# Kernel tuning notes

Measured on AMD Instinct MI355X. Metric: run time of the kernel, lower is better.

Reference implementation:

```python
import jax, jax.numpy as jnp
import numpy as np
import math

EMBED_DIM = 4096
NUM_HEADS = 32
NUM_KV_HEADS = 8
HEAD_DIM = EMBED_DIM // NUM_HEADS          # 128
GROUP_SIZE = NUM_HEADS // NUM_KV_HEADS     # 4
KV_DIM = EMBED_DIM // GROUP_SIZE           # 1024
BATCH, SEQ = 1, 2048


def softermax(x, axis=-1):
    # base-2 softmax with max subtraction (Softermax, arXiv:2103.09301)
    m = jnp.max(x, axis=axis, keepdims=True)
    p = jnp.exp2(x - m)
    return p / jnp.sum(p, axis=axis, keepdims=True)


def setup_inputs() -> dict:
    key = jax.random.key(0)
    ks = jax.random.split(key, 9)
    s = 1.0 / math.sqrt(EMBED_DIM)
    return {
        "x": jax.random.normal(ks[0], (BATCH, SEQ, EMBED_DIM), jnp.float32),
        "q_w": jax.random.normal(ks[1], (EMBED_DIM, EMBED_DIM), jnp.float32) * s,
        "q_b": jax.random.normal(ks[2], (EMBED_DIM,), jnp.float32) * s,
        "k_w": jax.random.normal(ks[3], (KV_DIM, EMBED_DIM), jnp.float32) * s,
        "k_b": jax.random.normal(ks[4], (KV_DIM,), jnp.float32) * s,
        "v_w": jax.random.normal(ks[5], (KV_DIM, EMBED_DIM), jnp.float32) * s,
        "v_b": jax.random.normal(ks[6], (KV_DIM,), jnp.float32) * s,
        "o_w": jax.random.normal(ks[7], (EMBED_DIM, EMBED_DIM), jnp.float32) * s,
        "o_b": jax.random.normal(ks[8], (EMBED_DIM,), jnp.float32) * s,
    }


def reference(x, q_w, q_b, k_w, k_b, v_w, v_b, o_w, o_b):
    B, S, E = x.shape
    # projections (torch Linear: y = x @ W.T + b)
    q = (x @ q_w.T + q_b).reshape(B, S, NUM_HEADS, HEAD_DIM).transpose(0, 2, 1, 3)   # [B,H,S,D]
    k = (x @ k_w.T + k_b).reshape(B, S, NUM_KV_HEADS, HEAD_DIM).transpose(0, 2, 1, 3)  # [B,KV,S,D]
    v = (x @ v_w.T + v_b).reshape(B, S, NUM_KV_HEADS, HEAD_DIM).transpose(0, 2, 1, 3)
    # repeat_kv: expand kv heads to num_heads
    k = jnp.repeat(k, GROUP_SIZE, axis=1)  # [B,H,S,D]
    v = jnp.repeat(v, GROUP_SIZE, axis=1)
    scale = 1.0 / math.sqrt(HEAD_DIM)
    attn = jnp.einsum("bhqd,bhkd->bhqk", q, k * scale)
    attn = softermax(attn, axis=-1)
    out = jnp.einsum("bhqk,bhkd->bhqd", attn, v)
    out = out.transpose(0, 2, 1, 3).reshape(B, S, E)
    return out @ o_w.T + o_b
```

## Files before the change

kernel.cpp:

```cpp
#include <hip/hip_runtime.h>
#include <hip/hip_bf16.h>
#include <stdint.h>

#define SEQL 2048
#define EMB 4096
#define KVDIM 1024
#define NHEADS 32
#define HD 128

typedef __attribute__((ext_vector_type(4))) float f32x4;
typedef __attribute__((ext_vector_type(8))) short bf16x8;
typedef unsigned short u16;
typedef unsigned int u32;

__device__ __forceinline__ u16 f2bf(float f) {
  u32 u = __builtin_bit_cast(u32, f);
  u = (u + 0x7FFFu + ((u >> 16) & 1u)) >> 16;
  return (u16)u;
}

__device__ __forceinline__ void gload_lds16(const void* g, void* l) {
  __builtin_amdgcn_global_load_lds(
      (const __attribute__((address_space(1))) void*)g,
      (__attribute__((address_space(3))) void*)l, 16, 0, 0);
}

__global__ __launch_bounds__(256) void k_convert(
    const float* __restrict__ x, const float* __restrict__ qw,
    const float* __restrict__ kw, const float* __restrict__ vw,
    const float* __restrict__ ow, u16* __restrict__ xb, u16* __restrict__ qwb,
    u16* __restrict__ kwb, u16* __restrict__ vwb, u16* __restrict__ owb) {
  const long NCH = 6291456;
  const long stride = (long)gridDim.x * 256;
  for (long c = (long)blockIdx.x * 256 + threadIdx.x; c < NCH; c += stride) {
    long i = c << 3;
    const float* s;
    u16* d;
    long off;
    if (i < 8388608) {
      s = x; d = xb; off = i;
    } else if (i < 25165824) {
      s = qw; d = qwb; off = i - 8388608;
    } else if (i < 29360128) {
      s = kw; d = kwb; off = i - 25165824;
    } else if (i < 33554432) {
      s = vw; d = vwb; off = i - 29360128;
    } else {
      s = ow; d = owb; off = i - 33554432;
    }
    float4 a = *(const float4*)(s + off);
    float4 b = *(const float4*)(s + off + 4);
    bf16x8 o;
    o[0] = f2bf(a.x); o[1] = f2bf(a.y); o[2] = f2bf(a.z); o[3] = f2bf(a.w);
    o[4] = f2bf(b.x); o[5] = f2bf(b.y); o[6] = f2bf(b.z); o[7] = f2bf(b.w);
    *(bf16x8*)(d + off) = o;
  }
}

__device__ __forceinline__ void gemm_core128(const u16* __restrict__ A,
                                             const u16* __restrict__ W, long m0,
                                             long n0, int lda, int ldb, int nkt,
                                             u16* sA, u16* sB, f32x4 acc[4][4]) {
  const int t = threadIdx.x, lane = t & 63, w = t >> 6;
  const int wr = w >> 1, wc = w & 1, r15 = lane & 15, kof = (lane >> 4) * 8;
  auto stage = [&](int buf, int kt) {
    const long k0 = (long)kt * 32;
#pragma unroll
    for (int i = 0; i < 2; ++i) {
      const int L = (i * 256 + t) * 8;
      gload_lds16(A + (m0 + (L >> 5)) * lda + k0 + (L & 31),
                  sA + buf * 4096 + i * 2048 + w * 512);
      gload_lds16(W + (n0 + (L >> 5)) * ldb + k0 + (L & 31),
                  sB + buf * 4096 + i * 2048 + w * 512);
    }
  };
  stage(0, 0);
  __syncthreads();
  int cur = 0;
  for (int kt = 0; kt < nkt; ++kt) {
    if (kt + 1 < nkt) stage(cur ^ 1, kt + 1);
    bf16x8 aF[4], bF[4];
#pragma unroll
    for (int m = 0; m < 4; ++m)
      aF[m] = *(const bf16x8*)(sA + cur * 4096 + (wr * 64 + m * 16 + r15) * 32 + kof);
#pragma unroll
    for (int n = 0; n < 4; ++n)
      bF[n] = *(const bf16x8*)(sB + cur * 4096 + (wc * 64 + n * 16 + r15) * 32 + kof);
#pragma unroll
    for (int m = 0; m < 4; ++m)
#pragma unroll
      for (int n = 0; n < 4; ++n)
        acc[m][n] =
            __builtin_amdgcn_mfma_f32_16x16x32_bf16(aF[m], bF[n], acc[m][n], 0, 0, 0);
    __syncthreads();
    cur ^= 1;
  }
}

__global__ __launch_bounds__(256, 2) void k_gemm_qkv(
    const u16* __restrict__ xb, const u16* __restrict__ qwb,
    const u16* __restrict__ kwb, const u16* __restrict__ vwb,
    const float* __restrict__ qb, const float* __restrict__ kb,
    const float* __restrict__ vb, u16* __restrict__ Q, u16* __restrict__ Kc,
    u16* __restrict__ Vt) {
  __shared__ u16 sA[2 * 4096];
  __shared__ u16 sB[2 * 4096];
  const int nt = blockIdx.x, mt = blockIdx.y;
  const u16* W;
  const float* bias;
  long n0;
  int mode;
  if (nt < 32) {
    W = qwb; bias = qb; n0 = (long)nt * 128; mode = 0;
  } else if (nt < 40) {
    W = kwb; bias = kb; n0 = (long)(nt - 32) * 128; mode = 1;
  } else {
    W = vwb; bias = vb; n0 = (long)(nt - 40) * 128; mode = 2;
  }
  const long m0 = (long)mt * 128;
  f32x4 acc[4][4] = {};
  gemm_core128(xb, W, m0, n0, EMB, EMB, 128, sA, sB, acc);
  const int lane = threadIdx.x & 63, w = threadIdx.x >> 6;
  const int wr = w >> 1, wc = w & 1, r15 = lane & 15, hi = lane >> 4;
#pragma unroll
  for (int n = 0; n < 4; ++n) {
    const long col = n0 + wc * 64 + n * 16 + r15;
    const float bv = bias[col];
#pragma unroll
    for (int m = 0; m < 4; ++m) {
#pragma unroll
      for (int i = 0; i < 4; ++i) {
        const long row = m0 + wr * 64 + m * 16 + hi * 4 + i;
        const float v = acc[m][n][i] + bv;
        if (mode == 0)
          Q[row * EMB + col] = f2bf(v);
        else if (mode == 1)
          Kc[row * KVDIM + col] = f2bf(v);
        else
          Vt[col * SEQL + row] = f2bf(v);
      }
    }
  }
}

__global__ __launch_bounds__(256, 2) void k_attn(const u16* __restrict__ Q,
                                                 const u16* __restrict__ Kc,
                                                 const u16* __restrict__ Vt,
                                                 u16* __restrict__ AO) {
  __shared__ u16 sK[64 * 128];
  __shared__ u16 sV[128 * 64];
  __shared__ u16 sP[4][32 * 72];
  const int h = blockIdx.y, kvh = h >> 2;
  const long q0 = (long)blockIdx.x * 128;
  const int t = threadIdx.x, lane = t & 63, w = t >> 6;
  const int r15 = lane & 15, hi = lane >> 4, kof = hi * 8;
  const float scale = 0.08838834764831845f;

  bf16x8 qf[2][4];
#pragma unroll
  for (int m = 0; m < 2; ++m)
#pragma unroll
    for (int ks = 0; ks < 4; ++ks)
      qf[m][ks] = *(const bf16x8*)(Q + (q0 + w * 32 + m * 16 + r15) * EMB +
                                   h * HD + ks * 32 + kof);

  f32x4 oacc[2][8] = {};
  float mx[2][4], sm[2][4];
#pragma unroll
  for (int m = 0; m < 2; ++m)
#pragma unroll
    for (int i = 0; i < 4; ++i) {
      mx[m][i] = -1e30f;
      sm[m][i] = 0.f;
    }

  for (int tk = 0; tk < 32; ++tk) {
    const long k0 = (long)tk * 64;
    __syncthreads();
#pragma unroll
    for (int i = 0; i < 4; ++i) {
      const int P = (i * 256 + t) * 16;
      const int row = P >> 8;
      const int cb = (P & 255) ^ ((row & 7) << 4);
      gload_lds16(Kc + (k0 + row) * KVDIM + kvh * HD + (cb >> 1),
                  (char*)sK + (i * 256 + w * 64) * 16);
      const int rowv = P >> 7;
      const int cbv = (P & 127) ^ ((rowv & 7) << 4);
      gload_lds16(Vt + (long)(kvh * HD + rowv) * SEQL + k0 + (cbv >> 1),
                  (char*)sV + (i * 256 + w * 64) * 16);
    }
    __syncthreads();
    f32x4 sacc[2][4] = {};
#pragma unroll
    for (int ks = 0; ks < 4; ++ks) {
      bf16x8 bF[4];
#pragma unroll
      for (int n = 0; n < 4; ++n) {
        const int row = n * 16 + r15;
        const int off = (row << 8) + (((ks * 32 + kof) << 1) ^ ((row & 7) << 4));
        bF[n] = *(const bf16x8*)((const char*)sK + off);
      }
#pragma unroll
      for (int m = 0; m < 2; ++m)
#pragma unroll
        for (int n = 0; n < 4; ++n)
          sacc[m][n] = __builtin_amdgcn_mfma_f32_16x16x32_bf16(qf[m][ks], bF[n],
                                                               sacc[m][n], 0, 0, 0);
    }
#pragma unroll
    for (int m = 0; m < 2; ++m) {
#pragma unroll
      for (int i = 0; i < 4; ++i) {
        float tmax = fmaxf(fmaxf(sacc[m][0][i], sacc[m][1][i]),
                           fmaxf(sacc[m][2][i], sacc[m][3][i]));
#pragma unroll
        for (int msk = 1; msk < 16; msk <<= 1)
          tmax = fmaxf(tmax, __shfl_xor(tmax, msk, 64));
        const float nm = fmaxf(mx[m][i], tmax * scale);
        const float corr = exp2f(mx[m][i] - nm);
        mx[m][i] = nm;
        sm[m][i] *= corr;
#pragma unroll
        for (int n = 0; n < 8; ++n) oacc[m][n][i] *= corr;
        float ps = 0.f;
#pragma unroll
        for (int n = 0; n < 4; ++n) {
          const float p = exp2f(sacc[m][n][i] * scale - nm);
          ps += p;
          sP[w][(m * 16 + hi * 4 + i) * 72 + n * 16 + r15] = f2bf(p);
        }
#pragma unroll
        for (int msk = 1; msk < 16; msk <<= 1) ps += __shfl_xor(ps, msk, 64);
        sm[m][i] += ps;
      }
    }
#pragma unroll
    for (int ks = 0; ks < 2; ++ks) {
      bf16x8 pF[2];
#pragma unroll
      for (int m = 0; m < 2; ++m)
        pF[m] = *(const bf16x8*)(&sP[w][(m * 16 + r15) * 72 + ks * 32 + kof]);
#pragma unroll
      for (int n = 0; n < 8; ++n) {
        const int row = n * 16 + r15;
        const int off = (row << 7) + (((ks * 32 + kof) << 1) ^ ((row & 7) << 4));
        const bf16x8 vF = *(const bf16x8*)((const char*)sV + off);
#pragma unroll
        for (int m = 0; m < 2; ++m)
          oacc[m][n] =
              __builtin_amdgcn_mfma_f32_16x16x32_bf16(pF[m], vF, oacc[m][n], 0, 0, 0);
      }
    }
  }
#pragma unroll
  for (int m = 0; m < 2; ++m) {
    float inv[4];
#pragma unroll
    for (int i = 0; i < 4; ++i) inv[i] = 1.f / sm[m][i];
#pragma unroll
    for (int n = 0; n < 8; ++n)
#pragma unroll
      for (int i = 0; i < 4; ++i)
        AO[(q0 + w * 32 + m * 16 + hi * 4 + i) * EMB + h * HD + n * 16 + r15] =
            f2bf(oacc[m][n][i] * inv[i]);
  }
}

__global__ __launch_bounds__(256, 2) void k_gemm_o(const u16* __restrict__ AO,
                                                   const u16* __restrict__ owb,
                                                   const float* __restrict__ ob,
                                                   float* __restrict__ OUT) {
  __shared__ u16 sA[2 * 4096];
  __shared__ u16 sB[2 * 4096];
  const long n0 = (long)blockIdx.x * 128, m0 = (long)blockIdx.y * 128;
  f32x4 acc[4][4] = {};
  gemm_core128(AO, owb, m0, n0, EMB, EMB, 128, sA, sB, acc);
  const int lane = threadIdx.x & 63, w = threadIdx.x >> 6;
  const int wr = w >> 1, wc = w & 1, r15 = lane & 15, hi = lane >> 4;
#pragma unroll
  for (int n = 0; n < 4; ++n) {
    const long col = n0 + wc * 64 + n * 16 + r15;
    const float bv = ob[col];
#pragma unroll
    for (int m = 0; m < 4; ++m) {
#pragma unroll
      for (int i = 0; i < 4; ++i) {
        const long row = m0 + wr * 64 + m * 16 + hi * 4 + i;
        OUT[row * EMB + col] = acc[m][n][i] + bv;
      }
    }
  }
}

extern "C" void kernel_launch(void* const* d_in, const int* in_sizes, int n_in,
                              void* d_out, int out_size, void* d_ws,
                              size_t ws_size, hipStream_t stream) {
  const float* x = (const float*)d_in[0];
  const float* qw = (const float*)d_in[1];
  const float* qb = (const float*)d_in[2];
  const float* kw = (const float*)d_in[3];
  const float* kb = (const float*)d_in[4];
  const float* vw = (const float*)d_in[5];
  const float* vb = (const float*)d_in[6];
  const float* ow = (const float*)d_in[7];
  const float* ob = (const float*)d_in[8];
  float* OUT = (float*)d_out;

  char* ws = (char*)d_ws;
  u16* xb = (u16*)ws;   ws += 16777216;
  u16* qwb = (u16*)ws;  ws += 33554432;
  u16* kwb = (u16*)ws;  ws += 8388608;
  u16* vwb = (u16*)ws;  ws += 8388608;
  u16* owb = (u16*)ws;  ws += 33554432;
  u16* Qb = (u16*)ws;   ws += 16777216;
  u16* Kb = (u16*)ws;   ws += 4194304;
  u16* Vtb = (u16*)ws;  ws += 4194304;
  u16* AO = (u16*)ws;   ws += 16777216;

  k_convert<<<2048, 256, 0, stream>>>(x, qw, kw, vw, ow, xb, qwb, kwb, vwb, owb);
  k_gemm_qkv<<<dim3(48, 16), 256, 0, stream>>>(xb, qwb, kwb, vwb, qb, kb, vb,
                                               Qb, Kb, Vtb);
  k_attn<<<dim3(16, 32), 256, 0, stream>>>(Qb, Kb, Vtb, AO);
  k_gemm_o<<<dim3(32, 16), 256, 0, stream>>>(AO, owb, ob, OUT);
}
```

Measured before the change: 586.2 us.

## Retile GEMMs to 128x256 with 512 threads and lazy-rescale attention

Both projection GEMMs move to a 128x256 tile on 512 threads. The new core uses K=64 steps, XOR-swizzled LDS, a two-stage global-to-LDS prefetch controlled by explicit vmcnt waits and raw barriers, and setprio around the MFMA bursts. Attention now gives each wave 16 query rows with 64-row blocks, doubling the grid, and raises occupancy to 3 blocks. It also rescales the softmax only when the tile max exceeds the running max by more than 8 (in log2 units), with the row-sum reduction deferred to the end. The aim is more data reuse per LDS load, better overlap of loads with compute, and less softmax overhead. The cost is higher register and LDS pressure, plus larger unnormalised exponentials.

```diff
diff --git a/kernel.cpp b/kernel.cpp
--- a/kernel.cpp
+++ b/kernel.cpp
@@ -5,7 +5,6 @@
 #define SEQL 2048
 #define EMB 4096
 #define KVDIM 1024
-#define NHEADS 32
 #define HD 128
 
 typedef __attribute__((ext_vector_type(4))) float f32x4;
@@ -57,71 +56,121 @@
   }
 }
 
-__device__ __forceinline__ void gemm_core128(const u16* __restrict__ A,
-                                             const u16* __restrict__ W, long m0,
-                                             long n0, int lda, int ldb, int nkt,
-                                             u16* sA, u16* sB, f32x4 acc[4][4]) {
-  const int t = threadIdx.x, lane = t & 63, w = t >> 6;
-  const int wr = w >> 1, wc = w & 1, r15 = lane & 15, kof = (lane >> 4) * 8;
+__device__ __forceinline__ void gemm_128x256(const u16* __restrict__ A,
+                                             const u16* __restrict__ B,
+                                             long aRow0, long bRow0, int lda,
+                                             int ldb, u16* sm, f32x4 acc[4][4]) {
+  const int t = threadIdx.x;
+  const int lane = t & 63, w = t >> 6;
+  const int wr = w >> 2, wc = w & 3;
+  const int r15 = lane & 15, hi = lane >> 4;
+  const int rsub = lane >> 3;
+  const int gofs = ((lane & 7) ^ rsub) << 3;
+  const int swz0 = ((0 + hi) ^ (r15 & 7)) << 4;
+  const int swz1 = ((4 + hi) ^ (r15 & 7)) << 4;
+
   auto stage = [&](int buf, int kt) {
-    const long k0 = (long)kt * 32;
+    const long k0 = (long)kt * 64 + gofs;
+    u16* base = sm + buf * 24576;
 #pragma unroll
     for (int i = 0; i < 2; ++i) {
-      const int L = (i * 256 + t) * 8;
-      gload_lds16(A + (m0 + (L >> 5)) * lda + k0 + (L & 31),
-                  sA + buf * 4096 + i * 2048 + w * 512);
-      gload_lds16(W + (n0 + (L >> 5)) * ldb + k0 + (L & 31),
-                  sB + buf * 4096 + i * 2048 + w * 512);
+      const int ch = i * 8 + w;
+      gload_lds16(A + (aRow0 + ch * 8 + rsub) * (long)lda + k0, base + ch * 512);
+    }
+#pragma unroll
+    for (int i = 0; i < 4; ++i) {
+      const int ch = i * 8 + w;
+      gload_lds16(B + (bRow0 + ch * 8 + rsub) * (long)ldb + k0,
+                  base + 8192 + ch * 512);
     }
   };
+
   stage(0, 0);
-  __syncthreads();
+  stage(1, 1);
+  asm volatile("s_waitcnt vmcnt(6)" ::: "memory");
+  __builtin_amdgcn_s_barrier();
+
+  const char* sc = (const char*)sm;
   int cur = 0;
-  for (int kt = 0; kt < nkt; ++kt) {
-    if (kt + 1 < nkt) stage(cur ^ 1, kt + 1);
-    bf16x8 aF[4], bF[4];
+  for (int kt = 0; kt < 64; ++kt) {
+    const char* base = sc + cur * 49152;
+    const char* aB = base + (wr * 64 + r15) * 128;
+    const char* bB = base + 16384 + (wc * 64 + r15) * 128;
+    bf16x8 aF[4][2], bF[2][2];
+#pragma unroll
+    for (int m = 0; m < 4; ++m) {
+      aF[m][0] = *(const bf16x8*)(aB + m * 2048 + swz0);
+      aF[m][1] = *(const bf16x8*)(aB + m * 2048 + swz1);
+    }
+#pragma unroll
+    for (int n = 0; n < 2; ++n) {
+      bF[n][0] = *(const bf16x8*)(bB + n * 2048 + swz0);
+      bF[n][1] = *(const bf16x8*)(bB + n * 2048 + swz1);
+    }
+    __builtin_amdgcn_s_setprio(1);
 #pragma unroll
     for (int m = 0; m < 4; ++m)
-      aF[m] = *(const bf16x8*)(sA + cur * 4096 + (wr * 64 + m * 16 + r15) * 32 + kof);
-#pragma unroll
-    for (int n = 0; n < 4; ++n)
-      bF[n] = *(const bf16x8*)(sB + cur * 4096 + (wc * 64 + n * 16 + r15) * 32 + kof);
+#pragma unroll
+      for (int n = 0; n < 2; ++n) {
+        acc[m][n] = __builtin_amdgcn_mfma_f32_16x16x32_bf16(aF[m][0], bF[n][0],
+                                                            acc[m][n], 0, 0, 0);
+        acc[m][n] = __builtin_amdgcn_mfma_f32_16x16x32_bf16(aF[m][1], bF[n][1],
+                                                            acc[m][n], 0, 0, 0);
+      }
+    __builtin_amdgcn_s_setprio(0);
+    bf16x8 cF[2][2];
+#pragma unroll
+    for (int n = 0; n < 2; ++n) {
+      cF[n][0] = *(const bf16x8*)(bB + (n + 2) * 2048 + swz0);
+      cF[n][1] = *(const bf16x8*)(bB + (n + 2) * 2048 + swz1);
+    }
+    __builtin_amdgcn_s_setprio(1);
 #pragma unroll
     for (int m = 0; m < 4; ++m)
 #pragma unroll
-      for (int n = 0; n < 4; ++n)
-        acc[m][n] =
-            __builtin_amdgcn_mfma_f32_16x16x32_bf16(aF[m], bF[n], acc[m][n], 0, 0, 0);
-    __syncthreads();
+      for (int n = 0; n < 2; ++n) {
+        acc[m][n + 2] = __builtin_amdgcn_mfma_f32_16x16x32_bf16(
+            aF[m][0], cF[n][0], acc[m][n + 2], 0, 0, 0);
+        acc[m][n + 2] = __builtin_amdgcn_mfma_f32_16x16x32_bf16(
+            aF[m][1], cF[n][1], acc[m][n + 2], 0, 0, 0);
+      }
+    __builtin_amdgcn_s_setprio(0);
+    __builtin_amdgcn_s_barrier();
+    if (kt + 2 < 64) {
+      stage(cur, kt + 2);
+      asm volatile("s_waitcnt vmcnt(6)" ::: "memory");
+    } else {
+      asm volatile("s_waitcnt vmcnt(0)" ::: "memory");
+    }
+    __builtin_amdgcn_s_barrier();
     cur ^= 1;
   }
 }
 
-__global__ __launch_bounds__(256, 2) void k_gemm_qkv(
+__global__ __launch_bounds__(512, 2) void k_gemm_qkv(
     const u16* __restrict__ xb, const u16* __restrict__ qwb,
     const u16* __restrict__ kwb, const u16* __restrict__ vwb,
     const float* __restrict__ qb, const float* __restrict__ kb,
     const float* __restrict__ vb, u16* __restrict__ Q, u16* __restrict__ Kc,
     u16* __restrict__ Vt) {
-  __shared__ u16 sA[2 * 4096];
-  __shared__ u16 sB[2 * 4096];
+  __shared__ u16 sm[49152];
   const int nt = blockIdx.x, mt = blockIdx.y;
   const u16* W;
   const float* bias;
   long n0;
   int mode;
-  if (nt < 32) {
-    W = qwb; bias = qb; n0 = (long)nt * 128; mode = 0;
-  } else if (nt < 40) {
-    W = kwb; bias = kb; n0 = (long)(nt - 32) * 128; mode = 1;
+  if (nt < 16) {
+    W = qwb; bias = qb; n0 = (long)nt * 256; mode = 0;
+  } else if (nt < 20) {
+    W = kwb; bias = kb; n0 = (long)(nt - 16) * 256; mode = 1;
   } else {
-    W = vwb; bias = vb; n0 = (long)(nt - 40) * 128; mode = 2;
+    W = vwb; bias = vb; n0 = (long)(nt - 20) * 256; mode = 2;
   }
   const long m0 = (long)mt * 128;
   f32x4 acc[4][4] = {};
-  gemm_core128(xb, W, m0, n0, EMB, EMB, 128, sA, sB, acc);
+  gemm_128x256(xb, W, m0, n0, EMB, EMB, sm, acc);
   const int lane = threadIdx.x & 63, w = threadIdx.x >> 6;
-  const int wr = w >> 1, wc = w & 1, r15 = lane & 15, hi = lane >> 4;
+  const int wr = w >> 2, wc = w & 3, r15 = lane & 15, hi = lane >> 4;
 #pragma unroll
   for (int n = 0; n < 4; ++n) {
     const long col = n0 + wc * 64 + n * 16 + r15;
@@ -129,9 +178,9 @@
 #pragma unroll
     for (int m = 0; m < 4; ++m) {
 #pragma unroll
-      for (int i = 0; i < 4; ++i) {
-        const long row = m0 + wr * 64 + m * 16 + hi * 4 + i;
-        const float v = acc[m][n][i] + bv;
+      for (int j = 0; j < 4; ++j) {
+        const long row = m0 + wr * 64 + m * 16 + hi * 4 + j;
+        const float v = acc[m][n][j] + bv;
         if (mode == 0)
           Q[row * EMB + col] = f2bf(v);
         else if (mode == 1)
@@ -143,36 +192,31 @@
   }
 }
 
-__global__ __launch_bounds__(256, 2) void k_attn(const u16* __restrict__ Q,
+__global__ __launch_bounds__(256, 3) void k_attn(const u16* __restrict__ Q,
                                                  const u16* __restrict__ Kc,
                                                  const u16* __restrict__ Vt,
                                                  u16* __restrict__ AO) {
   __shared__ u16 sK[64 * 128];
   __shared__ u16 sV[128 * 64];
-  __shared__ u16 sP[4][32 * 72];
+  __shared__ u16 sP[4][16 * 72];
   const int h = blockIdx.y, kvh = h >> 2;
-  const long q0 = (long)blockIdx.x * 128;
+  const long q0 = (long)blockIdx.x * 64;
   const int t = threadIdx.x, lane = t & 63, w = t >> 6;
   const int r15 = lane & 15, hi = lane >> 4, kof = hi * 8;
   const float scale = 0.08838834764831845f;
 
-  bf16x8 qf[2][4];
-#pragma unroll
-  for (int m = 0; m < 2; ++m)
-#pragma unroll
-    for (int ks = 0; ks < 4; ++ks)
-      qf[m][ks] = *(const bf16x8*)(Q + (q0 + w * 32 + m * 16 + r15) * EMB +
-                                   h * HD + ks * 32 + kof);
-
-  f32x4 oacc[2][8] = {};
-  float mx[2][4], sm[2][4];
-#pragma unroll
-  for (int m = 0; m < 2; ++m)
-#pragma unroll
-    for (int i = 0; i < 4; ++i) {
-      mx[m][i] = -1e30f;
-      sm[m][i] = 0.f;
-    }
+  bf16x8 qf[4];
+#pragma unroll
+  for (int ks = 0; ks < 4; ++ks)
+    qf[ks] = *(const bf16x8*)(Q + (q0 + w * 16 + r15) * EMB + h * HD + ks * 32 + kof);
+
+  f32x4 oacc[8] = {};
+  float mx[4], sms[4];
+#pragma unroll
+  for (int i = 0; i < 4; ++i) {
+    mx[i] = -1e30f;
+    sms[i] = 0.f;
+  }
 
   for (int tk = 0; tk < 32; ++tk) {
     const long k0 = (long)tk * 64;
@@ -190,7 +234,7 @@
                   (char*)sV + (i * 256 + w * 64) * 16);
     }
     __syncthreads();
-    f32x4 sacc[2][4] = {};
+    f32x4 sacc[4] = {};
 #pragma unroll
     for (int ks = 0; ks < 4; ++ks) {
       bf16x8 bF[4];
@@ -201,82 +245,73 @@
         bF[n] = *(const bf16x8*)((const char*)sK + off);
       }
 #pragma unroll
-      for (int m = 0; m < 2; ++m)
-#pragma unroll
-        for (int n = 0; n < 4; ++n)
-          sacc[m][n] = __builtin_amdgcn_mfma_f32_16x16x32_bf16(qf[m][ks], bF[n],
-                                                               sacc[m][n], 0, 0, 0);
-    }
-#pragma unroll
-    for (int m = 0; m < 2; ++m) {
-#pragma unroll
-      for (int i = 0; i < 4; ++i) {
-        float tmax = fmaxf(fmaxf(sacc[m][0][i], sacc[m][1][i]),
-                           fmaxf(sacc[m][2][i], sacc[m][3][i]));
+      for (int n = 0; n < 4; ++n)
+        sacc[n] = __builtin_amdgcn_mfma_f32_16x16x32_bf16(qf[ks], bF[n], sacc[n],
+                                                          0, 0, 0);
+    }
+#pragma unroll
+    for (int i = 0; i < 4; ++i) {
+      const float pm = fmaxf(fmaxf(sacc[0][i], sacc[1][i]),
+                             fmaxf(sacc[2][i], sacc[3][i]));
+      if (__any(pm * scale > mx[i] + 8.0f)) {
+        float tmax = pm;
 #pragma unroll
         for (int msk = 1; msk < 16; msk <<= 1)
           tmax = fmaxf(tmax, __shfl_xor(tmax, msk, 64));
-        const float nm = fmaxf(mx[m][i], tmax * scale);
-        const float corr = exp2f(mx[m][i] - nm);
-        mx[m][i] = nm;
-        sm[m][i] *= corr;
-#pragma unroll
-        for (int n = 0; n < 8; ++n) oacc[m][n][i] *= corr;
-        float ps = 0.f;
-#pragma unroll
-        for (int n = 0; n < 4; ++n) {
-          const float p = exp2f(sacc[m][n][i] * scale - nm);
-          ps += p;
-          sP[w][(m * 16 + hi * 4 + i) * 72 + n * 16 + r15] = f2bf(p);
-        }
-#pragma unroll
-        for (int msk = 1; msk < 16; msk <<= 1) ps += __shfl_xor(ps, msk, 64);
-        sm[m][i] += ps;
-      }
+        const float nm = fmaxf(mx[i], tmax * scale);
+        const float corr = exp2f(mx[i] - nm);
+        mx[i] = nm;
+        sms[i] *= corr;
+#pragma unroll
+        for (int n = 0; n < 8; ++n) oacc[n][i] *= corr;
+      }
+      float ps = 0.f;
+#pragma unroll
+      for (int n = 0; n < 4; ++n) {
+        const float p = exp2f(sacc[n][i] * scale - mx[i]);
+        ps += p;
+        sP[w][(hi * 4 + i) * 72 + n * 16 + r15] = f2bf(p);
+      }
+      sms[i] += ps;
     }
 #pragma unroll
     for (int ks = 0; ks < 2; ++ks) {
-      bf16x8 pF[2];
-#pragma unroll
-      for (int m = 0; m < 2; ++m)
-        pF[m] = *(const bf16x8*)(&sP[w][(m * 16 + r15) * 72 + ks * 32 + kof]);
+      const bf16x8 pF = *(const bf16x8*)(&sP[w][r15 * 72 + ks * 32 + kof]);
 #pragma unroll
       for (int n = 0; n < 8; ++n) {
         const int row = n * 16 + r15;
         const int off = (row << 7) + (((ks * 32 + kof) << 1) ^ ((row & 7) << 4));
         const bf16x8 vF = *(const bf16x8*)((const char*)sV + off);
-#pragma unroll
-        for (int m = 0; m < 2; ++m)
-          oacc[m][n] =
-              __builtin_amdgcn_mfma_f32_16x16x32_bf16(pF[m], vF, oacc[m][n], 0, 0, 0);
-      }
-    }
-  }
-#pragma unroll
-  for (int m = 0; m < 2; ++m) {
-    float inv[4];
-#pragma unroll
-    for (int i = 0; i < 4; ++i) inv[i] = 1.f / sm[m][i];
-#pragma unroll
-    for (int n = 0; n < 8; ++n)
-#pragma unroll
-      for (int i = 0; i < 4; ++i)
-        AO[(q0 + w * 32 + m * 16 + hi * 4 + i) * EMB + h * HD + n * 16 + r15] =
-            f2bf(oacc[m][n][i] * inv[i]);
-  }
-}
-
-__global__ __launch_bounds__(256, 2) void k_gemm_o(const u16* __restrict__ AO,
+        oacc[n] = __builtin_amdgcn_mfma_f32_16x16x32_bf16(pF, vF, oacc[n], 0, 0, 0);
+      }
+    }
+  }
+  float inv[4];
+#pragma unroll
+  for (int i = 0; i < 4; ++i) {
+    float s = sms[i];
+#pragma unroll
+    for (int msk = 1; msk < 16; msk <<= 1) s += __shfl_xor(s, msk, 64);
+    inv[i] = 1.f / s;
+  }
+#pragma unroll
+  for (int n = 0; n < 8; ++n)
+#pragma unroll
+    for (int i = 0; i < 4; ++i)
+      AO[(q0 + w * 16 + hi * 4 + i) * EMB + h * HD + n * 16 + r15] =
+          f2bf(oacc[n][i] * inv[i]);
+}
+
+__global__ __launch_bounds__(512, 2) void k_gemm_o(const u16* __restrict__ AO,
                                                    const u16* __restrict__ owb,
                                                    const float* __restrict__ ob,
                                                    float* __restrict__ OUT) {
-  __shared__ u16 sA[2 * 4096];
-  __shared__ u16 sB[2 * 4096];
-  const long n0 = (long)blockIdx.x * 128, m0 = (long)blockIdx.y * 128;
+  __shared__ u16 sm[49152];
+  const long n0 = (long)blockIdx.x * 256, m0 = (long)blockIdx.y * 128;
   f32x4 acc[4][4] = {};
-  gemm_core128(AO, owb, m0, n0, EMB, EMB, 128, sA, sB, acc);
+  gemm_128x256(AO, owb, m0, n0, EMB, EMB, sm, acc);
   const int lane = threadIdx.x & 63, w = threadIdx.x >> 6;
-  const int wr = w >> 1, wc = w & 1, r15 = lane & 15, hi = lane >> 4;
+  const int wr = w >> 2, wc = w & 3, r15 = lane & 15, hi = lane >> 4;
 #pragma unroll
   for (int n = 0; n < 4; ++n) {
     const long col = n0 + wc * 64 + n * 16 + r15;
@@ -284,9 +319,9 @@
 #pragma unroll
     for (int m = 0; m < 4; ++m) {
 #pragma unroll
-      for (int i = 0; i < 4; ++i) {
-        const long row = m0 + wr * 64 + m * 16 + hi * 4 + i;
-        OUT[row * EMB + col] = acc[m][n][i] + bv;
+      for (int j = 0; j < 4; ++j) {
+        const long row = m0 + wr * 64 + m * 16 + hi * 4 + j;
+        OUT[row * EMB + col] = acc[m][n][j] + bv;
       }
     }
   }
@@ -318,8 +353,8 @@
   u16* AO = (u16*)ws;   ws += 16777216;
 
   k_convert<<<2048, 256, 0, stream>>>(x, qw, kw, vw, ow, xb, qwb, kwb, vwb, owb);
-  k_gemm_qkv<<<dim3(48, 16), 256, 0, stream>>>(xb, qwb, kwb, vwb, qb, kb, vb,
+  k_gemm_qkv<<<dim3(24, 16), 512, 0, stream>>>(xb, qwb, kwb, vwb, qb, kb, vb,
                                                Qb, Kb, Vtb);
-  k_attn<<<dim3(16, 32), 256, 0, stream>>>(Qb, Kb, Vtb, AO);
-  k_gemm_o<<<dim3(32, 16), 256, 0, stream>>>(AO, owb, ob, OUT);
-}
+  k_attn<<<dim3(32, 32), 256, 0, stream>>>(Qb, Kb, Vtb, AO);
+  k_gemm_o<<<dim3(16, 16), 512, 0, stream>>>(AO, owb, ob, OUT);
+}
```

New measurement: 575.0 us. About the same (-1.9%).
